# Performance work log

Measured on AMD Instinct MI355X. Metric: run time of the kernel, lower is better.

## Reference

```python
import jax, jax.numpy as jnp
import numpy as np

B, N, D_MODEL = 4, 4096, 1024
HEADS, DIM_HEAD = 16, 64
HIDDEN = HEADS * DIM_HEAD
SCALE = DIM_HEAD ** -0.5


def setup_inputs() -> dict:
    key = jax.random.key(0)
    k1, k2, k3, k4 = jax.random.split(key, 4)
    x = jax.random.normal(k1, (B, N, D_MODEL), dtype=jnp.float32)
    w_qkv = jax.random.normal(k2, (D_MODEL, 3 * HIDDEN), dtype=jnp.float32) * (D_MODEL ** -0.5)
    w_out = jax.random.normal(k3, (HIDDEN, D_MODEL), dtype=jnp.float32) * (HIDDEN ** -0.5)
    b_out = jax.random.normal(k4, (D_MODEL,), dtype=jnp.float32) * 0.01
    return {"x": x, "w_qkv": w_qkv, "w_out": w_out, "b_out": b_out}


def reference(x, w_qkv, w_out, b_out):
    b, n, _ = x.shape
    qkv = x @ w_qkv  # [b, n, 3*hidden]
    q, k, v = jnp.split(qkv, 3, axis=-1)

    def to_bhdn(t):
        # 'b n (h d) -> b h d n'
        return t.reshape(b, n, HEADS, DIM_HEAD).transpose(0, 2, 3, 1)

    q, k, v = map(to_bhdn, (q, k, v))
    q = jax.nn.softmax(q, axis=-2) * SCALE  # softmax over feature dim d
    k = jax.nn.softmax(k, axis=-1)          # softmax over sequence dim n
    context = jnp.einsum('bhdn,bhen->bhde', k, v)  # [b,h,d,e], d=e=dim_head
    out = jnp.einsum('bhde,bhdn->bhen', context, q)
    # 'b h e n -> b n (h e)'
    out = out.transpose(0, 3, 1, 2).reshape(b, n, HIDDEN)
    return out @ w_out + b_out
```

## Files before the change

### kernel.cpp

```cpp
#include <hip/hip_runtime.h>
#include <hip/hip_bf16.h>


typedef unsigned short u16t;
typedef __bf16 bf16x8 __attribute__((ext_vector_type(8)));
typedef float f32x4 __attribute__((ext_vector_type(4)));
typedef unsigned short ushort8 __attribute__((ext_vector_type(8)));

__device__ __forceinline__ u16t f2bf(float f) {
    union { float f; unsigned int u; } v; v.f = f;
    unsigned int r = v.u + 0x7fffu + ((v.u >> 16) & 1u);
    return (u16t)(r >> 16);
}
__device__ __forceinline__ float bf2f(u16t h) {
    union { unsigned int u; float f; } v; v.u = ((unsigned int)h) << 16;
    return v.f;
}

#define GLOAD_LDS16(gptr, lptr) \
    __builtin_amdgcn_global_load_lds((const __attribute__((address_space(1))) unsigned int*)(gptr), \
                                     (__attribute__((address_space(3))) unsigned int*)(lptr), 16, 0, 0)
#define SFENCE asm volatile("" ::: "memory")

__global__ __launch_bounds__(256) void prep_kernel(const float* __restrict__ x, u16t* __restrict__ xb,
                                                   const float* __restrict__ w_qkv, u16t* __restrict__ wqkvT,
                                                   const float* __restrict__ w_out, u16t* __restrict__ woutT) {
    int bid = blockIdx.x, t = threadIdx.x;
    if (bid < 2048) {
        int i = (bid * 256 + t) * 4;
        for (; i < 16777216; i += 2048 * 256 * 4) {
            float4 v = *(const float4*)(x + i);
            ushort4 o;
            o.x = f2bf(v.x); o.y = f2bf(v.y); o.z = f2bf(v.z); o.w = f2bf(v.w);
            *(ushort4*)(xb + i) = o;
        }
        return;
    }
    __shared__ float tile[32][33];
    const float* in; u16t* out; int R, C, bx, by;
    if (bid < 5120) { in = w_qkv; out = wqkvT; R = 1024; C = 3072; int b2 = bid - 2048; bx = b2 % 96; by = b2 / 96; }
    else            { in = w_out; out = woutT; R = 1024; C = 1024; int b3 = bid - 5120; bx = b3 & 31; by = b3 >> 5; }
    int c0 = bx * 32, r0 = by * 32;
    int tx = t & 31, ty = t >> 5;
    for (int i = 0; i < 32; i += 8)
        tile[ty + i][tx] = in[(size_t)(r0 + ty + i) * C + c0 + tx];
    __syncthreads();
    for (int i = 0; i < 32; i += 8)
        out[(size_t)(c0 + ty + i) * R + r0 + tx] = f2bf(tile[tx][ty + i]);
}

template<int OUTF32, int BIAS, int BATCHB, int KSUM>
__device__ __forceinline__ void gemm256_body(const u16t* __restrict__ A, const u16t* __restrict__ Bt,
                                             void* __restrict__ Cout, const float* __restrict__ bias,
                                             float* __restrict__ ksum,
                                             int M, int N, int K, int NBX, int lda) {
    __shared__ __align__(16) u16t lds[65536];
    const int t = threadIdx.x;
    const int l = t & 63, w = t >> 6;
    const int wm = w >> 2, wn = w & 3;

    int cpx = gridDim.x >> 3;
    int wg = ((int)blockIdx.x & 7) * cpx + ((int)blockIdx.x >> 3);
    int bx = wg % NBX, by = wg / NBX;
    const int m0 = by * 256, n0 = bx * 256;
    const int NT = K >> 6;
    if (BATCHB) Bt += (size_t)(by >> 4) << 20;

    const int colk0 = ((l >> 4) ^ (l & 7)) * 8;
    const int colk1 = colk0 ^ 32;
    const int abase = (wm * 32 + (l & 15)) * 64;
    const int bbase = 16384 + (wn >> 1) * 8192 + ((wn & 1) * 64 + (l & 15)) * 64;

    const int rr = w * 8 + (l >> 3);
    const int coloff = ((l ^ (l >> 3)) & 7) * 8;
    const int rowA = rr + ((rr >= 32) ? 96 : 0);
    const u16t* pa_st = A  + (size_t)(m0 + rowA) * lda + coloff;
    const u16t* pb_st = Bt + (size_t)(n0 + rr) * K + coloff;
    const int so = w * 512;

#define SPAIR(qq, kto, pb) do { \
    size_t k64_ = (size_t)(kto) * 64; \
    if ((qq) == 0) { \
        GLOAD_LDS16(pb_st + k64_,                  &lds[(pb) * 32768 + 16384 + so]); \
        GLOAD_LDS16(pb_st + k64_ + (size_t)64 * K, &lds[(pb) * 32768 + 20480 + so]); \
    } else if ((qq) == 1) { \
        GLOAD_LDS16(pb_st + k64_ + (size_t)128 * K, &lds[(pb) * 32768 + 24576 + so]); \
        GLOAD_LDS16(pb_st + k64_ + (size_t)192 * K, &lds[(pb) * 32768 + 28672 + so]); \
    } else if ((qq) == 2) { \
        GLOAD_LDS16(pa_st + k64_,                    &lds[(pb) * 32768 + so]); \
        GLOAD_LDS16(pa_st + k64_ + (size_t)32 * lda, &lds[(pb) * 32768 + 4096 + so]); \
    } else { \
        GLOAD_LDS16(pa_st + k64_ + (size_t)64 * lda, &lds[(pb) * 32768 + 8192 + so]); \
        GLOAD_LDS16(pa_st + k64_ + (size_t)96 * lda, &lds[(pb) * 32768 + 12288 + so]); \
    } \
} while (0)

    f32x4 acc[8][4] = {};

    SPAIR(0, 0, 0); SPAIR(1, 0, 0); SPAIR(2, 0, 0);
    SFENCE;
    SPAIR(3, 0, 0);

    for (int kt = 0; kt < NT; ++kt) {
        const int p = kt & 1;
        const bool sn = (kt + 1 < NT);
        const u16t* lA = &lds[p * 32768];

        asm volatile("s_waitcnt vmcnt(2)" ::: "memory");
        __builtin_amdgcn_s_barrier();

        bf16x8 bfr[4][2];
#pragma unroll
        for (int ni = 0; ni < 4; ++ni) {
            bfr[ni][0] = *(const bf16x8*)&lA[bbase + ni * 1024 + colk0];
            bfr[ni][1] = *(const bf16x8*)&lA[bbase + ni * 1024 + colk1];
        }
        bf16x8 af1[2][2][2];
#pragma unroll
        for (int g = 0; g < 2; ++g) {
            af1[g][0][0] = *(const bf16x8*)&lA[g * 4096 + abase + colk0];
            af1[g][0][1] = *(const bf16x8*)&lA[g * 4096 + abase + colk1];
            af1[g][1][0] = *(const bf16x8*)&lA[g * 4096 + abase + 1024 + colk0];
            af1[g][1][1] = *(const bf16x8*)&lA[g * 4096 + abase + 1024 + colk1];
        }
        if (sn) { SPAIR(0, kt + 1, p ^ 1); SPAIR(1, kt + 1, p ^ 1); SPAIR(2, kt + 1, p ^ 1); }
        __builtin_amdgcn_s_setprio(1);
#pragma unroll
        for (int g = 0; g < 2; ++g)
#pragma unroll
            for (int dm = 0; dm < 2; ++dm)
#pragma unroll
                for (int ni = 0; ni < 4; ++ni)
#pragma unroll
                    for (int kk = 0; kk < 2; ++kk)
                        acc[g * 2 + dm][ni] = __builtin_amdgcn_mfma_f32_16x16x32_bf16(
                            af1[g][dm][kk], bfr[ni][kk], acc[g * 2 + dm][ni], 0, 0, 0);
        __builtin_amdgcn_s_setprio(0);

        if (sn) asm volatile("s_waitcnt vmcnt(6)" ::: "memory");
        else    asm volatile("s_waitcnt vmcnt(0)" ::: "memory");
        __builtin_amdgcn_s_barrier();

        bf16x8 af2[2][2][2];
#pragma unroll
        for (int g = 0; g < 2; ++g) {
            af2[g][0][0] = *(const bf16x8*)&lA[(g + 2) * 4096 + abase + colk0];
            af2[g][0][1] = *(const bf16x8*)&lA[(g + 2) * 4096 + abase + colk1];
            af2[g][1][0] = *(const bf16x8*)&lA[(g + 2) * 4096 + abase + 1024 + colk0];
            af2[g][1][1] = *(const bf16x8*)&lA[(g + 2) * 4096 + abase + 1024 + colk1];
        }
        if (sn) SPAIR(3, kt + 1, p ^ 1);
        __builtin_amdgcn_s_setprio(1);
#pragma unroll
        for (int g = 0; g < 2; ++g)
#pragma unroll
            for (int dm = 0; dm < 2; ++dm)
#pragma unroll
                for (int ni = 0; ni < 4; ++ni)
#pragma unroll
                    for (int kk = 0; kk < 2; ++kk)
                        acc[4 + g * 2 + dm][ni] = __builtin_amdgcn_mfma_f32_16x16x32_bf16(
                            af2[g][dm][kk], bfr[ni][kk], acc[4 + g * 2 + dm][ni], 0, 0, 0);
        __builtin_amdgcn_s_setprio(0);
    }
#undef SPAIR

    if (KSUM && n0 >= 1024 && n0 < 2048) {
#pragma unroll
        for (int ni = 0; ni < 4; ++ni) {
            float se = 0.f;
#pragma unroll
            for (int mi = 0; mi < 8; ++mi)
#pragma unroll
                for (int j = 0; j < 4; ++j)
                    se += __expf(acc[mi][ni][j]);
            se += __shfl_xor(se, 16);
            se += __shfl_xor(se, 32);
            if ((l >> 4) == 0)
                atomicAdd(&ksum[(by >> 4) * 1024 + (n0 - 1024) + wn * 64 + ni * 16 + l], se);
        }
    }

#pragma unroll
    for (int mi = 0; mi < 8; ++mi) {
        int row = m0 + wm * 128 + mi * 16 + ((l >> 4) << 2);
#pragma unroll
        for (int ni = 0; ni < 4; ++ni) {
            int col = n0 + wn * 64 + ni * 16 + (l & 15);
            float bv = BIAS ? bias[col] : 0.f;
#pragma unroll
            for (int j = 0; j < 4; ++j) {
                float v = acc[mi][ni][j] + bv;
                if (OUTF32) ((float*)Cout)[(size_t)(row + j) * N + col] = v;
                else        ((u16t*)Cout)[(size_t)(row + j) * N + col] = f2bf(v);
            }
        }
    }
}

__global__ __launch_bounds__(512, 2) void gemm_qkv(const u16t* __restrict__ A, const u16t* __restrict__ Bt,
                                                   u16t* __restrict__ C, float* __restrict__ ksum) {
    gemm256_body<0, 0, 0, 1>(A, Bt, C, nullptr, ksum, 16384, 3072, 1024, 12, 1024);
}

__global__ __launch_bounds__(512, 2) void gemm_out(const u16t* __restrict__ A, const u16t* __restrict__ Bt,
                                                   float* __restrict__ C, const float* __restrict__ bias) {
    gemm256_body<1, 1, 1, 0>(A, Bt, C, bias, nullptr, 16384, 1024, 1024, 4, 3072);
}

__global__ __launch_bounds__(256) void post_qkv(u16t* __restrict__ qkv,
                                                const float* __restrict__ ksum,
                                                float* __restrict__ ctxT) {
    int bid = blockIdx.x, t = threadIdx.x;
    if (bid < 512) {
        int bh = bid >> 3, chunk = bid & 7;
        int b = bh >> 4, h = bh & 15;
        __shared__ u16t kT[64 * 136];
        __shared__ u16t vT[64 * 136];
        int lane = t & 63, w = t >> 6;
        f32x4 acc[4] = {};
        for (int sub = 0; sub < 4; sub++) {
            size_t rowbase = ((size_t)b * 4096 + chunk * 512 + sub * 128) * 3072 + h * 64;
#pragma unroll
            for (int i = 0; i < 4; i++) {
                int P = t + 256 * i;
                int n = P >> 3, c = P & 7;
                size_t ro = rowbase + (size_t)n * 3072 + c * 8;
                ushort8 k8 = *(const ushort8*)(&qkv[ro + 1024]);
                ushort8 v8 = *(const ushort8*)(&qkv[ro + 2048]);
                int nx = n ^ (c << 3);
#pragma unroll
                for (int j = 0; j < 8; j++) {
                    kT[(c * 8 + j) * 136 + nx] = f2bf(__expf(bf2f(k8[j])));
                    vT[(c * 8 + j) * 136 + nx] = v8[j];
                }
            }
            __syncthreads();
#pragma unroll
            for (int ks = 0; ks < 4; ks++) {
                int er = w * 16 + (lane & 15);
                int nb = ks * 32 + ((lane >> 4) << 3);
                bf16x8 a = *(const bf16x8*)(&vT[er * 136 + (nb ^ ((er >> 3) << 3))]);
#pragma unroll
                for (int ct = 0; ct < 4; ct++) {
                    int dr = ct * 16 + (lane & 15);
                    bf16x8 bb = *(const bf16x8*)(&kT[dr * 136 + (nb ^ ((dr >> 3) << 3))]);
                    acc[ct] = __builtin_amdgcn_mfma_f32_16x16x32_bf16(a, bb, acc[ct], 0, 0, 0);
                }
            }
            __syncthreads();
        }
#pragma unroll
        for (int ct = 0; ct < 4; ct++) {
            int e = w * 16 + ((lane >> 4) << 2);
            int dd = ct * 16 + (lane & 15);
            float gi = 1.0f / ksum[b * 1024 + h * 64 + dd];
#pragma unroll
            for (int j = 0; j < 4; j++)
                atomicAdd(&ctxT[(size_t)bh * 4096 + (e + j) * 64 + dd], acc[ct][j] * gi);
        }
        return;
    }
    int qb = bid - 512;
#pragma unroll
    for (int it = 0; it < 8; ++it) {
        int r = qb * 256 + it * 32 + (t >> 3);
        size_t addr = (size_t)(r >> 4) * 3072 + (r & 15) * 64 + (t & 7) * 8;
        ushort8 ch = *(const ushort8*)(&qkv[addr]);
        float v0 = bf2f(ch[0]), v1 = bf2f(ch[1]), v2 = bf2f(ch[2]), v3 = bf2f(ch[3]);
        float v4 = bf2f(ch[4]), v5 = bf2f(ch[5]), v6 = bf2f(ch[6]), v7 = bf2f(ch[7]);
        float m = fmaxf(fmaxf(fmaxf(v0, v1), fmaxf(v2, v3)), fmaxf(fmaxf(v4, v5), fmaxf(v6, v7)));
        m = fmaxf(m, __shfl_xor(m, 1)); m = fmaxf(m, __shfl_xor(m, 2)); m = fmaxf(m, __shfl_xor(m, 4));
        float e0 = __expf(v0 - m), e1 = __expf(v1 - m), e2 = __expf(v2 - m), e3 = __expf(v3 - m);
        float e4 = __expf(v4 - m), e5 = __expf(v5 - m), e6 = __expf(v6 - m), e7 = __expf(v7 - m);
        float s = e0 + e1 + e2 + e3 + e4 + e5 + e6 + e7;
        s += __shfl_xor(s, 1); s += __shfl_xor(s, 2); s += __shfl_xor(s, 4);
        float inv = 0.125f / s;
        ushort8 o;
        o[0] = f2bf(e0 * inv); o[1] = f2bf(e1 * inv); o[2] = f2bf(e2 * inv); o[3] = f2bf(e3 * inv);
        o[4] = f2bf(e4 * inv); o[5] = f2bf(e5 * inv); o[6] = f2bf(e6 * inv); o[7] = f2bf(e7 * inv);
        *(ushort8*)(&qkv[addr]) = o;
    }
}

__global__ __launch_bounds__(256) void w2_kernel(const float* __restrict__ ctxT,
                                                 const u16t* __restrict__ woutT,
                                                 u16t* __restrict__ w2t) {
    int bh = blockIdx.x, jc = blockIdx.y;
    int b = bh >> 4, h = bh & 15;
    __shared__ u16t cb[64][72];
    __shared__ u16t wl[256][72];
    int t = threadIdx.x;
#pragma unroll
    for (int i = 0; i < 16; i++) {
        int f = t + 256 * i;
        cb[f & 63][f >> 6] = f2bf(ctxT[(size_t)bh * 4096 + f]);
    }
#pragma unroll
    for (int i = 0; i < 8; i++) {
        int f = t + 256 * i;
        int r = f >> 3, q = f & 7;
        *(uint4*)(&wl[r][q * 8]) = *(const uint4*)(&woutT[(size_t)(jc * 256 + r) * 1024 + h * 64 + q * 8]);
    }
    __syncthreads();
    int l = t & 63, w = t >> 6;
    f32x4 acc[4][4] = {};
#pragma unroll
    for (int kk = 0; kk < 2; kk++) {
        bf16x8 af[4], bfr[4];
#pragma unroll
        for (int mt = 0; mt < 4; mt++)
            af[mt] = *(const bf16x8*)&wl[w * 64 + mt * 16 + (l & 15)][(l >> 4) * 8 + kk * 32];
#pragma unroll
        for (int nt = 0; nt < 4; nt++)
            bfr[nt] = *(const bf16x8*)&cb[nt * 16 + (l & 15)][(l >> 4) * 8 + kk * 32];
#pragma unroll
        for (int mt = 0; mt < 4; mt++)
#pragma unroll
            for (int nt = 0; nt < 4; nt++)
                acc[mt][nt] = __builtin_amdgcn_mfma_f32_16x16x32_bf16(af[mt], bfr[nt], acc[mt][nt], 0, 0, 0);
    }
#pragma unroll
    for (int mt = 0; mt < 4; mt++) {
        int j = jc * 256 + w * 64 + mt * 16 + ((l >> 4) << 2);
#pragma unroll
        for (int nt = 0; nt < 4; nt++) {
            int dd = nt * 16 + (l & 15);
#pragma unroll
            for (int jj = 0; jj < 4; jj++)
                w2t[((size_t)b << 20) + (size_t)(j + jj) * 1024 + h * 64 + dd] = f2bf(acc[mt][nt][jj]);
        }
    }
}


extern "C" void kernel_launch(void* const* d_in, const int* in_sizes, int n_in,
                              void* d_out, int out_size, void* d_ws, size_t ws_size,
                              hipStream_t stream) {
    const float* x     = (const float*)d_in[0];
    const float* w_qkv = (const float*)d_in[1];
    const float* w_out = (const float*)d_in[2];
    const float* b_out = (const float*)d_in[3];
    float* out = (float*)d_out;
    char* ws = (char*)d_ws;

    size_t o_xb    = 0;
    size_t o_wqkvT = 33554432;
    size_t o_woutT = 39845888;
    size_t o_qkv   = 41943040;
    size_t o_ctx   = 142606336;
    size_t o_ksum  = 143654912;
    size_t needed  = 143720448;
    if (ws_size < needed) return;

    u16t* xb     = (u16t*)(ws + o_xb);
    u16t* w2t    = (u16t*)(ws + o_xb);
    u16t* wqkvT  = (u16t*)(ws + o_wqkvT);
    u16t* woutT  = (u16t*)(ws + o_woutT);
    u16t* qkvb   = (u16t*)(ws + o_qkv);
    float* ctxT  = (float*)(ws + o_ctx);
    float* ksum  = (float*)(ws + o_ksum);

    hipMemsetAsync(ksum, 0, 65536, stream);
    hipMemsetAsync(ctxT, 0, 64 * 64 * 64 * 4, stream);

    prep_kernel<<<6144, 256, 0, stream>>>(x, xb, w_qkv, wqkvT, w_out, woutT);

    gemm_qkv<<<768, 512, 0, stream>>>(xb, wqkvT, qkvb, ksum);

    post_qkv<<<1536, 256, 0, stream>>>(qkvb, ksum, ctxT);

    w2_kernel<<<dim3(64, 4), 256, 0, stream>>>(ctxT, woutT, w2t);

    gemm_out<<<256, 512, 0, stream>>>(qkvb, w2t, out, b_out);
}
```

Baseline: 201.5 us.

## Load GEMM B operand directly to registers from a k8-interleaved layout

The weight operands for both GEMMs are now stored in a k-blocked layout ([K/8][N][8]), so each lane can load its B fragments straight from global memory into registers. Only A is staged through LDS, which halves LDS use and simplifies the pipeline to one barrier per k-tile with register double-buffering of B. The two memsets are folded into extra blocks of the prep kernel, and w2_kernel writes its output through LDS to get coalesced 16-byte stores. The trade-off is that B is now fetched redundantly from global or L2 by every wave, and the loop waits on vmcnt(0) each iteration, giving up the finer-grained overlap the old schedule had.

Result: slower. 386.0 us (+91.5%).

```diff
diff --git a/kernel.cpp b/kernel.cpp
--- a/kernel.cpp
+++ b/kernel.cpp
@@ -20,11 +20,11 @@
 #define GLOAD_LDS16(gptr, lptr) \
     __builtin_amdgcn_global_load_lds((const __attribute__((address_space(1))) unsigned int*)(gptr), \
                                      (__attribute__((address_space(3))) unsigned int*)(lptr), 16, 0, 0)
-#define SFENCE asm volatile("" ::: "memory")
 
 __global__ __launch_bounds__(256) void prep_kernel(const float* __restrict__ x, u16t* __restrict__ xb,
-                                                   const float* __restrict__ w_qkv, u16t* __restrict__ wqkvT,
-                                                   const float* __restrict__ w_out, u16t* __restrict__ woutT) {
+                                                   const float* __restrict__ w_qkv, u16t* __restrict__ wqkvB2,
+                                                   const float* __restrict__ w_out, u16t* __restrict__ woutT,
+                                                   float* __restrict__ zbase) {
     int bid = blockIdx.x, t = threadIdx.x;
     if (bid < 2048) {
         int i = (bid * 256 + t) * 4;
@@ -36,25 +36,46 @@
         }
         return;
     }
-    __shared__ float tile[32][33];
-    const float* in; u16t* out; int R, C, bx, by;
-    if (bid < 5120) { in = w_qkv; out = wqkvT; R = 1024; C = 3072; int b2 = bid - 2048; bx = b2 % 96; by = b2 / 96; }
-    else            { in = w_out; out = woutT; R = 1024; C = 1024; int b3 = bid - 5120; bx = b3 & 31; by = b3 >> 5; }
-    int c0 = bx * 32, r0 = by * 32;
-    int tx = t & 31, ty = t >> 5;
-    for (int i = 0; i < 32; i += 8)
-        tile[ty + i][tx] = in[(size_t)(r0 + ty + i) * C + c0 + tx];
-    __syncthreads();
-    for (int i = 0; i < 32; i += 8)
-        out[(size_t)(c0 + ty + i) * R + r0 + tx] = f2bf(tile[tx][ty + i]);
-}
-
-template<int OUTF32, int BIAS, int BATCHB, int KSUM>
-__device__ __forceinline__ void gemm256_body(const u16t* __restrict__ A, const u16t* __restrict__ Bt,
+    if (bid >= 6144) {
+        float4* z = (float4*)zbase;
+        int i = (bid - 6144) * 256 + t;
+        for (; i < 69632; i += 68 * 256) z[i] = make_float4(0.f, 0.f, 0.f, 0.f);
+        return;
+    }
+    if (bid < 5120) {
+        int b2 = bid - 2048;
+        int k0 = (b2 / 96) * 32, n0 = (b2 % 96) * 32;
+        __shared__ float tile[32][33];
+        int tx = t & 31, ty = t >> 5;
+        for (int i = 0; i < 32; i += 8)
+            tile[ty + i][tx] = w_qkv[(size_t)(k0 + ty + i) * 3072 + n0 + tx];
+        __syncthreads();
+        if (ty < 4) {
+            ushort8 o;
+#pragma unroll
+            for (int j = 0; j < 8; j++) o[j] = f2bf(tile[ty * 8 + j][tx]);
+            *(ushort8*)(&wqkvB2[((size_t)((k0 >> 3) + ty) * 3072 + n0 + tx) * 8]) = o;
+        }
+        return;
+    }
+    {
+        int b3 = bid - 5120;
+        int c0 = (b3 & 31) * 32, r0 = (b3 >> 5) * 32;
+        __shared__ float tile[32][33];
+        int tx = t & 31, ty = t >> 5;
+        for (int i = 0; i < 32; i += 8)
+            tile[ty + i][tx] = w_out[(size_t)(r0 + ty + i) * 1024 + c0 + tx];
+        __syncthreads();
+        for (int i = 0; i < 32; i += 8)
+            woutT[(size_t)(c0 + ty + i) * 1024 + r0 + tx] = f2bf(tile[tx][ty + i]);
+    }
+}
+
+template<int OUTF32, int BIAS, int BATCHB, int KSUM, int NC>
+__device__ __forceinline__ void gemm256_body(const u16t* __restrict__ A, const u16t* __restrict__ B2,
                                              void* __restrict__ Cout, const float* __restrict__ bias,
-                                             float* __restrict__ ksum,
-                                             int M, int N, int K, int NBX, int lda) {
-    __shared__ __align__(16) u16t lds[65536];
+                                             float* __restrict__ ksum, int N, int NBX, int lda) {
+    __shared__ __align__(16) u16t lds[32768];
     const int t = threadIdx.x;
     const int l = t & 63, w = t >> 6;
     const int wm = w >> 2, wn = w & 3;
@@ -63,107 +84,80 @@
     int wg = ((int)blockIdx.x & 7) * cpx + ((int)blockIdx.x >> 3);
     int bx = wg % NBX, by = wg / NBX;
     const int m0 = by * 256, n0 = bx * 256;
-    const int NT = K >> 6;
-    if (BATCHB) Bt += (size_t)(by >> 4) << 20;
+    if (BATCHB) B2 += (size_t)(by >> 4) << 20;
 
     const int colk0 = ((l >> 4) ^ (l & 7)) * 8;
     const int colk1 = colk0 ^ 32;
     const int abase = (wm * 32 + (l & 15)) * 64;
-    const int bbase = 16384 + (wn >> 1) * 8192 + ((wn & 1) * 64 + (l & 15)) * 64;
 
     const int rr = w * 8 + (l >> 3);
     const int coloff = ((l ^ (l >> 3)) & 7) * 8;
     const int rowA = rr + ((rr >= 32) ? 96 : 0);
-    const u16t* pa_st = A  + (size_t)(m0 + rowA) * lda + coloff;
-    const u16t* pb_st = Bt + (size_t)(n0 + rr) * K + coloff;
+    const u16t* pa_st = A + (size_t)(m0 + rowA) * lda + coloff;
     const int so = w * 512;
 
-#define SPAIR(qq, kto, pb) do { \
+    const int bcol = n0 + wn * 64 + (l & 15);
+    const int ccl = l >> 4;
+
+#define ASTAGE(kto, pb) do { \
     size_t k64_ = (size_t)(kto) * 64; \
-    if ((qq) == 0) { \
-        GLOAD_LDS16(pb_st + k64_,                  &lds[(pb) * 32768 + 16384 + so]); \
-        GLOAD_LDS16(pb_st + k64_ + (size_t)64 * K, &lds[(pb) * 32768 + 20480 + so]); \
-    } else if ((qq) == 1) { \
-        GLOAD_LDS16(pb_st + k64_ + (size_t)128 * K, &lds[(pb) * 32768 + 24576 + so]); \
-        GLOAD_LDS16(pb_st + k64_ + (size_t)192 * K, &lds[(pb) * 32768 + 28672 + so]); \
-    } else if ((qq) == 2) { \
-        GLOAD_LDS16(pa_st + k64_,                    &lds[(pb) * 32768 + so]); \
-        GLOAD_LDS16(pa_st + k64_ + (size_t)32 * lda, &lds[(pb) * 32768 + 4096 + so]); \
-    } else { \
-        GLOAD_LDS16(pa_st + k64_ + (size_t)64 * lda, &lds[(pb) * 32768 + 8192 + so]); \
-        GLOAD_LDS16(pa_st + k64_ + (size_t)96 * lda, &lds[(pb) * 32768 + 12288 + so]); \
+    GLOAD_LDS16(pa_st + k64_,                    &lds[(pb) * 16384 + so]); \
+    GLOAD_LDS16(pa_st + k64_ + (size_t)32 * lda, &lds[(pb) * 16384 + 4096 + so]); \
+    GLOAD_LDS16(pa_st + k64_ + (size_t)64 * lda, &lds[(pb) * 16384 + 8192 + so]); \
+    GLOAD_LDS16(pa_st + k64_ + (size_t)96 * lda, &lds[(pb) * 16384 + 12288 + so]); \
+} while (0)
+
+#define BLOAD(kto, breg) do { \
+    _Pragma("unroll") \
+    for (int ni = 0; ni < 4; ++ni) \
+        _Pragma("unroll") \
+        for (int kk = 0; kk < 2; ++kk) \
+            breg[ni][kk] = *(const bf16x8*)&B2[((size_t)((kto) * 8 + kk * 4 + ccl) * NC + bcol + ni * 16) * 8]; \
+} while (0)
+
+#define TILE_BODY(kt, p, bCur, bNxt) do { \
+    if ((kt) + 1 < 16) { BLOAD((kt) + 1, bNxt); ASTAGE((kt) + 1, (p) ^ 1); } \
+    const u16t* lA = &lds[(p) * 16384]; \
+    bf16x8 af[4][2][2]; \
+    _Pragma("unroll") \
+    for (int g = 0; g < 4; ++g) { \
+        af[g][0][0] = *(const bf16x8*)&lA[g * 4096 + abase + colk0]; \
+        af[g][0][1] = *(const bf16x8*)&lA[g * 4096 + abase + colk1]; \
+        af[g][1][0] = *(const bf16x8*)&lA[g * 4096 + abase + 1024 + colk0]; \
+        af[g][1][1] = *(const bf16x8*)&lA[g * 4096 + abase + 1024 + colk1]; \
     } \
+    __builtin_amdgcn_s_setprio(1); \
+    _Pragma("unroll") \
+    for (int g = 0; g < 4; ++g) \
+        _Pragma("unroll") \
+        for (int dm = 0; dm < 2; ++dm) \
+            _Pragma("unroll") \
+            for (int ni = 0; ni < 4; ++ni) \
+                _Pragma("unroll") \
+                for (int kk = 0; kk < 2; ++kk) \
+                    acc[g * 2 + dm][ni] = __builtin_amdgcn_mfma_f32_16x16x32_bf16( \
+                        af[g][dm][kk], bCur[ni][kk], acc[g * 2 + dm][ni], 0, 0, 0); \
+    __builtin_amdgcn_s_setprio(0); \
+    asm volatile("s_waitcnt vmcnt(0)" ::: "memory"); \
+    __builtin_amdgcn_s_barrier(); \
 } while (0)
 
     f32x4 acc[8][4] = {};
-
-    SPAIR(0, 0, 0); SPAIR(1, 0, 0); SPAIR(2, 0, 0);
-    SFENCE;
-    SPAIR(3, 0, 0);
-
-    for (int kt = 0; kt < NT; ++kt) {
-        const int p = kt & 1;
-        const bool sn = (kt + 1 < NT);
-        const u16t* lA = &lds[p * 32768];
-
-        asm volatile("s_waitcnt vmcnt(2)" ::: "memory");
-        __builtin_amdgcn_s_barrier();
-
-        bf16x8 bfr[4][2];
-#pragma unroll
-        for (int ni = 0; ni < 4; ++ni) {
-            bfr[ni][0] = *(const bf16x8*)&lA[bbase + ni * 1024 + colk0];
-            bfr[ni][1] = *(const bf16x8*)&lA[bbase + ni * 1024 + colk1];
-        }
-        bf16x8 af1[2][2][2];
-#pragma unroll
-        for (int g = 0; g < 2; ++g) {
-            af1[g][0][0] = *(const bf16x8*)&lA[g * 4096 + abase + colk0];
-            af1[g][0][1] = *(const bf16x8*)&lA[g * 4096 + abase + colk1];
-            af1[g][1][0] = *(const bf16x8*)&lA[g * 4096 + abase + 1024 + colk0];
-            af1[g][1][1] = *(const bf16x8*)&lA[g * 4096 + abase + 1024 + colk1];
-        }
-        if (sn) { SPAIR(0, kt + 1, p ^ 1); SPAIR(1, kt + 1, p ^ 1); SPAIR(2, kt + 1, p ^ 1); }
-        __builtin_amdgcn_s_setprio(1);
-#pragma unroll
-        for (int g = 0; g < 2; ++g)
-#pragma unroll
-            for (int dm = 0; dm < 2; ++dm)
-#pragma unroll
-                for (int ni = 0; ni < 4; ++ni)
-#pragma unroll
-                    for (int kk = 0; kk < 2; ++kk)
-                        acc[g * 2 + dm][ni] = __builtin_amdgcn_mfma_f32_16x16x32_bf16(
-                            af1[g][dm][kk], bfr[ni][kk], acc[g * 2 + dm][ni], 0, 0, 0);
-        __builtin_amdgcn_s_setprio(0);
-
-        if (sn) asm volatile("s_waitcnt vmcnt(6)" ::: "memory");
-        else    asm volatile("s_waitcnt vmcnt(0)" ::: "memory");
-        __builtin_amdgcn_s_barrier();
-
-        bf16x8 af2[2][2][2];
-#pragma unroll
-        for (int g = 0; g < 2; ++g) {
-            af2[g][0][0] = *(const bf16x8*)&lA[(g + 2) * 4096 + abase + colk0];
-            af2[g][0][1] = *(const bf16x8*)&lA[(g + 2) * 4096 + abase + colk1];
-            af2[g][1][0] = *(const bf16x8*)&lA[(g + 2) * 4096 + abase + 1024 + colk0];
-            af2[g][1][1] = *(const bf16x8*)&lA[(g + 2) * 4096 + abase + 1024 + colk1];
-        }
-        if (sn) SPAIR(3, kt + 1, p ^ 1);
-        __builtin_amdgcn_s_setprio(1);
-#pragma unroll
-        for (int g = 0; g < 2; ++g)
-#pragma unroll
-            for (int dm = 0; dm < 2; ++dm)
-#pragma unroll
-                for (int ni = 0; ni < 4; ++ni)
-#pragma unroll
-                    for (int kk = 0; kk < 2; ++kk)
-                        acc[4 + g * 2 + dm][ni] = __builtin_amdgcn_mfma_f32_16x16x32_bf16(
-                            af2[g][dm][kk], bfr[ni][kk], acc[4 + g * 2 + dm][ni], 0, 0, 0);
-        __builtin_amdgcn_s_setprio(0);
-    }
-#undef SPAIR
+    bf16x8 bE[4][2], bO[4][2];
+
+    ASTAGE(0, 0);
+    BLOAD(0, bE);
+    asm volatile("s_waitcnt vmcnt(0)" ::: "memory");
+    __builtin_amdgcn_s_barrier();
+
+#pragma unroll
+    for (int k2 = 0; k2 < 8; ++k2) {
+        TILE_BODY(2 * k2,     0, bE, bO);
+        TILE_BODY(2 * k2 + 1, 1, bO, bE);
+    }
+#undef TILE_BODY
+#undef BLOAD
+#undef ASTAGE
 
     if (KSUM && n0 >= 1024 && n0 < 2048) {
 #pragma unroll
@@ -198,14 +192,14 @@
     }
 }
 
-__global__ __launch_bounds__(512, 2) void gemm_qkv(const u16t* __restrict__ A, const u16t* __restrict__ Bt,
+__global__ __launch_bounds__(512, 2) void gemm_qkv(const u16t* __restrict__ A, const u16t* __restrict__ B2,
                                                    u16t* __restrict__ C, float* __restrict__ ksum) {
-    gemm256_body<0, 0, 0, 1>(A, Bt, C, nullptr, ksum, 16384, 3072, 1024, 12, 1024);
-}
-
-__global__ __launch_bounds__(512, 2) void gemm_out(const u16t* __restrict__ A, const u16t* __restrict__ Bt,
+    gemm256_body<0, 0, 0, 1, 3072>(A, B2, C, nullptr, ksum, 3072, 12, 1024);
+}
+
+__global__ __launch_bounds__(512, 2) void gemm_out(const u16t* __restrict__ A, const u16t* __restrict__ B2,
                                                    float* __restrict__ C, const float* __restrict__ bias) {
-    gemm256_body<1, 1, 1, 0>(A, Bt, C, bias, nullptr, 16384, 1024, 1024, 4, 3072);
+    gemm256_body<1, 1, 1, 0, 1024>(A, B2, C, bias, nullptr, 1024, 4, 3072);
 }
 
 __global__ __launch_bounds__(256) void post_qkv(u16t* __restrict__ qkv,
@@ -320,16 +314,25 @@
             for (int nt = 0; nt < 4; nt++)
                 acc[mt][nt] = __builtin_amdgcn_mfma_f32_16x16x32_bf16(af[mt], bfr[nt], acc[mt][nt], 0, 0, 0);
     }
+    __syncthreads();
 #pragma unroll
     for (int mt = 0; mt < 4; mt++) {
-        int j = jc * 256 + w * 64 + mt * 16 + ((l >> 4) << 2);
+        int jl = w * 64 + mt * 16 + ((l >> 4) << 2);
 #pragma unroll
         for (int nt = 0; nt < 4; nt++) {
             int dd = nt * 16 + (l & 15);
 #pragma unroll
             for (int jj = 0; jj < 4; jj++)
-                w2t[((size_t)b << 20) + (size_t)(j + jj) * 1024 + h * 64 + dd] = f2bf(acc[mt][nt][jj]);
-        }
+                wl[jl + jj][dd] = f2bf(acc[mt][nt][jj]);
+        }
+    }
+    __syncthreads();
+#pragma unroll
+    for (int i = 0; i < 8; i++) {
+        int idx = t + 256 * i;
+        int j = idx & 255, cc = idx >> 8;
+        ushort8 o = *(const ushort8*)(&wl[j][cc * 8]);
+        *(ushort8*)(&w2t[((size_t)b << 20) + ((size_t)(h * 8 + cc) * 1024 + jc * 256 + j) * 8]) = o;
     }
 }
 
@@ -355,18 +358,15 @@
 
     u16t* xb     = (u16t*)(ws + o_xb);
     u16t* w2t    = (u16t*)(ws + o_xb);
-    u16t* wqkvT  = (u16t*)(ws + o_wqkvT);
+    u16t* wqkvB2 = (u16t*)(ws + o_wqkvT);
     u16t* woutT  = (u16t*)(ws + o_woutT);
     u16t* qkvb   = (u16t*)(ws + o_qkv);
     float* ctxT  = (float*)(ws + o_ctx);
     float* ksum  = (float*)(ws + o_ksum);
 
-    hipMemsetAsync(ksum, 0, 65536, stream);
-    hipMemsetAsync(ctxT, 0, 64 * 64 * 64 * 4, stream);
-
-    prep_kernel<<<6144, 256, 0, stream>>>(x, xb, w_qkv, wqkvT, w_out, woutT);
-
-    gemm_qkv<<<768, 512, 0, stream>>>(xb, wqkvT, qkvb, ksum);
+    prep_kernel<<<6212, 256, 0, stream>>>(x, xb, w_qkv, wqkvB2, w_out, woutT, ctxT);
+
+    gemm_qkv<<<768, 512, 0, stream>>>(xb, wqkvB2, qkvb, ksum);
 
     post_qkv<<<1536, 256, 0, stream>>>(qkvb, ksum, ctxT);
 
```
